# Optimization experiments

Measured on AMD Instinct MI355X. Metric: run time of the kernel, lower is better.

The kernel has to match this reference:

```python
import jax, jax.numpy as jnp
import numpy as np

K = 2  # top-k experts per token

def setup_inputs() -> dict:
    key = jax.random.key(0)
    ks = jax.random.split(key, 4)
    B, D, E, H = 8192, 512, 8, 2048
    x = jax.random.normal(ks[0], (B, D), dtype=jnp.float32)
    w_gate = jax.random.normal(ks[1], (D, E), dtype=jnp.float32) * 0.02
    W1 = jax.random.normal(ks[2], (E, D, H), dtype=jnp.float32) * (1.0 / np.sqrt(D))
    b1 = jnp.zeros((E, H), dtype=jnp.float32)
    W2 = jax.random.normal(ks[3], (E, H, D), dtype=jnp.float32) * (1.0 / np.sqrt(H))
    b2 = jnp.zeros((E, D), dtype=jnp.float32)
    return {"x": x, "w_gate": w_gate, "W1": W1, "b1": b1, "W2": W2, "b2": b2}

def reference(x, w_gate, W1, b1, W2, b2):
    B, E = x.shape[0], w_gate.shape[1]
    # --- gating (eval path: clean logits, no noise) ---
    logits = x @ w_gate                                  # [B, E]
    top_vals, top_idx = jax.lax.top_k(logits, K)         # [B, K]
    top_gates = jax.nn.softmax(top_vals, axis=-1)        # softmax over top-k logits
    rows = jnp.arange(B)[:, None]
    gates = jnp.zeros((B, E), dtype=x.dtype).at[rows, top_idx].set(top_gates)  # [B, E]
    # --- expert MLPs (grouped GEMMs) ---
    h = jax.nn.gelu(jnp.einsum('bd,edh->beh', x, W1) + b1[None], approximate=False)  # [B, E, H]
    out = jnp.einsum('beh,ehd->bed', h, W2) + b2[None]   # [B, E, D]
    # --- combine weighted by sparse gates ---
    y = jnp.einsum('be,bed->bd', gates, out)             # [B, D]
    return y
```

## Files before the change

kernel.cpp:

```cpp
#include <hip/hip_runtime.h>
#include <cstdint>

#define B_TOK 8192
#define DIM   512
#define NEXP  8
#define HID   2048

#define BM 128
#define BN 128
#define BK 64
#define BN2 64

typedef float  floatx4 __attribute__((ext_vector_type(4)));
typedef __bf16 bf16x8  __attribute__((ext_vector_type(8)));

__device__ __forceinline__ unsigned short f2bf(float f){
  unsigned u = __float_as_uint(f);
  u += 0x7fffu + ((u >> 16) & 1u);
  return (unsigned short)(u >> 16);
}

__device__ __forceinline__ float gelu_exact(float v){
  return 0.5f * v * (1.0f + erff(v * 0.70710678118654752440f));
}

__device__ __forceinline__ void async_load16(const void* g, void* l){
  __builtin_amdgcn_global_load_lds(
      (__attribute__((address_space(1))) unsigned int*)const_cast<void*>(g),
      (__attribute__((address_space(3))) unsigned int*)l, 16, 0, 0);
}


__global__ void k_cvt_x(const float* __restrict__ x, unsigned short* __restrict__ xb){
  int i = blockIdx.x * blockDim.x + threadIdx.x;
  float4 v = ((const float4*)x)[i];
  ushort4 o;
  o.x = f2bf(v.x); o.y = f2bf(v.y); o.z = f2bf(v.z); o.w = f2bf(v.w);
  ((ushort4*)xb)[i] = o;
}

__global__ __launch_bounds__(256)
void k_transpose_bf16(const float* __restrict__ src, unsigned short* __restrict__ dst,
                      int R, int C){
  __shared__ unsigned short tile[64][65];
  const size_t eoff = (size_t)blockIdx.z * (size_t)R * (size_t)C;
  const float* s = src + eoff;
  unsigned short* d = dst + eoff;
  int r0 = blockIdx.y * 64, c0 = blockIdx.x * 64;
  int tr = threadIdx.x >> 4, tc = threadIdx.x & 15;
  #pragma unroll
  for (int i = 0; i < 4; i++){
    int r = tr + i * 16;
    float4 v = *(const float4*)(s + (size_t)(r0 + r) * C + c0 + tc * 4);
    tile[tc*4+0][r] = f2bf(v.x);
    tile[tc*4+1][r] = f2bf(v.y);
    tile[tc*4+2][r] = f2bf(v.z);
    tile[tc*4+3][r] = f2bf(v.w);
  }
  __syncthreads();
  #pragma unroll
  for (int i = 0; i < 4; i++){
    int rr = tr + i * 16;
    ushort4 o;
    o.x = tile[rr][tc*4+0]; o.y = tile[rr][tc*4+1];
    o.z = tile[rr][tc*4+2]; o.w = tile[rr][tc*4+3];
    *(ushort4*)(d + (size_t)(c0 + rr) * R + r0 + tc * 4) = o;
  }
}

__global__ __launch_bounds__(256)
void k_gate(const float* __restrict__ x, const float* __restrict__ wg,
            int* __restrict__ tidx, float* __restrict__ tgate){
  const int wave = threadIdx.x >> 6, lane = threadIdx.x & 63;
  const int t = blockIdx.x * 4 + wave;
  const float* xr = x + (size_t)t * DIM;
  double acc[8];
  #pragma unroll
  for (int e = 0; e < 8; e++) acc[e] = 0.0;
  for (int d = lane; d < DIM; d += 64){
    double xv = (double)xr[d];
    float4 a = *(const float4*)(wg + d * 8);
    float4 b = *(const float4*)(wg + d * 8 + 4);
    acc[0] += xv * (double)a.x; acc[1] += xv * (double)a.y;
    acc[2] += xv * (double)a.z; acc[3] += xv * (double)a.w;
    acc[4] += xv * (double)b.x; acc[5] += xv * (double)b.y;
    acc[6] += xv * (double)b.z; acc[7] += xv * (double)b.w;
  }
  #pragma unroll
  for (int off = 32; off > 0; off >>= 1){
    #pragma unroll
    for (int e = 0; e < 8; e++)
      acc[e] += __shfl_down(acc[e], off);
  }
  if (lane == 0){
    int i0 = 0; double v0 = acc[0];
    #pragma unroll
    for (int e = 1; e < 8; e++) if (acc[e] > v0){ v0 = acc[e]; i0 = e; }
    int i1 = -1; double v1 = -1e300;
    #pragma unroll
    for (int e = 0; e < 8; e++) if (e != i0 && acc[e] > v1){ v1 = acc[e]; i1 = e; }
    double g0 = 1.0 / (1.0 + exp(v1 - v0));
    tidx[2*t]   = i0; tidx[2*t+1] = i1;
    tgate[2*t]  = (float)g0;
    tgate[2*t+1]= (float)(1.0 - g0);
  }
}

__global__ __launch_bounds__(1024)
void k_count(const int* __restrict__ tidx, int* __restrict__ ctrl){
  __shared__ int hist[16][8];
  const int tid = threadIdx.x;
  const int wave = tid >> 6;
  if (tid < 128) ((int*)hist)[tid] = 0;
  __syncthreads();
  #pragma unroll
  for (int i = 0; i < 8; i++){
    int t = i * 1024 + tid;
    int2 e = ((const int2*)tidx)[t];
    atomicAdd(&hist[wave][e.x], 1);
    atomicAdd(&hist[wave][e.y], 1);
  }
  __syncthreads();
  if (tid == 0){
    int o = 0;
    for (int e = 0; e < 8; e++){
      int c = 0;
      for (int w = 0; w < 16; w++) c += hist[w][e];
      ctrl[e] = c; ctrl[8 + e] = o; ctrl[16 + e] = o; o += c;
    }
  }
}

__global__ __launch_bounds__(256)
void k_place(const int* __restrict__ tidx, int* __restrict__ ctrl,
             int* __restrict__ perm, int2* __restrict__ slotpos){
  __shared__ int cnt[8];
  __shared__ int base[8];
  const int tid = threadIdx.x;
  if (tid < 8) cnt[tid] = 0;
  __syncthreads();
  const int t = blockIdx.x * 256 + tid;
  const int e0 = tidx[2*t], e1 = tidx[2*t+1];
  const int r0 = atomicAdd(&cnt[e0], 1);
  const int r1 = atomicAdd(&cnt[e1], 1);
  __syncthreads();
  if (tid < 8) base[tid] = atomicAdd(&ctrl[16 + tid], cnt[tid]);
  __syncthreads();
  const int p0 = base[e0] + r0, p1 = base[e1] + r1;
  perm[p0] = t;
  perm[p1] = t;
  slotpos[t] = make_int2(p0, p1);
}

__global__ __launch_bounds__(256, 2)
void k_gemm1(const unsigned short* __restrict__ xb,
             const unsigned short* __restrict__ w1t,
             const float* __restrict__ b1,
             unsigned short* __restrict__ h,
             const int* __restrict__ perm,
             const int* __restrict__ ctrl){
  const int e = blockIdx.z;
  const int count = ctrl[e];
  const int m0 = blockIdx.x * BM;
  if (m0 >= count) return;
  const int hoff = ctrl[8 + e];
  const int n0 = blockIdx.y * BN;

  __shared__ unsigned short smem[BM*BK + BN*BK + 2048];
  unsigned short* As = smem;
  unsigned short* Bs = smem + BM*BK;

  const int tid  = threadIdx.x;
  const int wave = tid >> 6;
  const int lane = tid & 63;
  const int rl   = wave * 32 + (lane >> 3);
  const int swz  = (lane & 7) ^ ((lane >> 3) & 7);

  const unsigned short* agp[4];
  const unsigned short* bgp[4];
  const unsigned short* w1e = w1t + (size_t)e * HID * DIM;
  #pragma unroll
  for (int i = 0; i < 4; i++){
    int mrow = m0 + rl + i * 8;
    int cl = mrow < count ? mrow : count - 1;
    int srow = perm[hoff + cl];
    agp[i] = xb + (size_t)srow * DIM + swz * 8;
    bgp[i] = w1e + (size_t)(n0 + rl + i * 8) * DIM + swz * 8;
  }
  unsigned short* asw = As + (wave * 32) * BK + lane * 8;
  unsigned short* bsw = Bs + (wave * 32) * BK + lane * 8;

  const int mh = (wave & 1) * 64;
  const int nh = (wave >> 1) * 64;
  const int fr = lane & 15;
  const int fq = lane >> 4;

  floatx4 acc[4][4];
  floatx4 zero = {0.f, 0.f, 0.f, 0.f};
  #pragma unroll
  for (int i = 0; i < 4; i++)
    #pragma unroll
    for (int j = 0; j < 4; j++) acc[i][j] = zero;

  for (int kt = 0; kt < DIM / BK; ++kt){
    #pragma unroll
    for (int i = 0; i < 4; i++){
      async_load16(agp[i] + kt * BK, asw + i * 8 * BK);
      async_load16(bgp[i] + kt * BK, bsw + i * 8 * BK);
    }
    __syncthreads();
    #pragma unroll
    for (int ks = 0; ks < 2; ks++){
      bf16x8 af[4], bfv[4];
      int kc = ks * 4 + fq;
      #pragma unroll
      for (int i = 0; i < 4; i++){
        int row = mh + i * 16 + fr;
        af[i] = *(const bf16x8*)(As + row * BK + ((kc ^ (row & 7)) << 3));
      }
      #pragma unroll
      for (int j = 0; j < 4; j++){
        int row = nh + j * 16 + fr;
        bfv[j] = *(const bf16x8*)(Bs + row * BK + ((kc ^ (row & 7)) << 3));
      }
      #pragma unroll
      for (int i = 0; i < 4; i++)
        #pragma unroll
        for (int j = 0; j < 4; j++)
          acc[i][j] = __builtin_amdgcn_mfma_f32_16x16x32_bf16(af[i], bfv[j], acc[i][j], 0, 0, 0);
    }
    __syncthreads();
  }

  unsigned short* wr = smem + wave * 4608;
  const int cm = fq * 4;
  const float* b1e = b1 + e * HID;
  #pragma unroll
  for (int i = 0; i < 4; i++){
    #pragma unroll
    for (int j = 0; j < 4; j++){
      float bias = b1e[n0 + nh + j * 16 + fr];
      #pragma unroll
      for (int r = 0; r < 4; r++){
        float v = acc[i][j][r] + bias;
        wr[(i * 16 + cm + r) * 72 + j * 16 + fr] = f2bf(gelu_exact(v));
      }
    }
  }
  __syncthreads();
  #pragma unroll
  for (int it = 0; it < 8; ++it){
    int row = it * 8 + (lane >> 3);
    int mrow = m0 + mh + row;
    if (mrow < count){
      uint4 vv = *(const uint4*)(wr + row * 72 + (lane & 7) * 8);
      *(uint4*)(h + (size_t)(hoff + mrow) * HID + n0 + nh + (lane & 7) * 8) = vv;
    }
  }
}

__global__ __launch_bounds__(256, 4)
void k_gemm2(const unsigned short* __restrict__ h,
             const unsigned short* __restrict__ w2t,
             float* __restrict__ slots,
             const int* __restrict__ ctrl){
  const int e = blockIdx.z;
  const int count = ctrl[e];
  const int m0 = blockIdx.x * BM;
  if (m0 >= count) return;
  const int hoff = ctrl[8 + e];
  const int n0 = blockIdx.y * BN2;

  __shared__ unsigned short smem[BM*BK + BN2*BK];
  unsigned short* As = smem;
  unsigned short* Bs = smem + BM*BK;

  const int tid  = threadIdx.x;
  const int wave = tid >> 6;
  const int lane = tid & 63;
  const int rl   = wave * 32 + (lane >> 3);
  const int rlb  = wave * 16 + (lane >> 3);
  const int swz  = (lane & 7) ^ ((lane >> 3) & 7);

  const unsigned short* agp[4];
  const unsigned short* bgp[2];
  const unsigned short* w2e = w2t + (size_t)e * DIM * HID;
  #pragma unroll
  for (int i = 0; i < 4; i++){
    agp[i] = h + (size_t)(hoff + m0 + rl + i * 8) * HID + swz * 8;
  }
  #pragma unroll
  for (int i = 0; i < 2; i++){
    bgp[i] = w2e + (size_t)(n0 + rlb + i * 8) * HID + swz * 8;
  }
  unsigned short* asw = As + (wave * 32) * BK + lane * 8;
  unsigned short* bsw = Bs + (wave * 16) * BK + lane * 8;

  const int mh  = (wave & 1) * 64;
  const int nh2 = (wave >> 1) * 32;
  const int fr = lane & 15;
  const int fq = lane >> 4;

  floatx4 acc[4][2];
  floatx4 zero = {0.f, 0.f, 0.f, 0.f};
  #pragma unroll
  for (int i = 0; i < 4; i++)
    #pragma unroll
    for (int j = 0; j < 2; j++) acc[i][j] = zero;

  for (int kt = 0; kt < HID / BK; ++kt){
    #pragma unroll
    for (int i = 0; i < 4; i++)
      async_load16(agp[i] + kt * BK, asw + i * 8 * BK);
    #pragma unroll
    for (int i = 0; i < 2; i++)
      async_load16(bgp[i] + kt * BK, bsw + i * 8 * BK);
    __syncthreads();
    #pragma unroll
    for (int ks = 0; ks < 2; ks++){
      bf16x8 af[4], bfv[2];
      int kc = ks * 4 + fq;
      #pragma unroll
      for (int i = 0; i < 4; i++){
        int row = mh + i * 16 + fr;
        af[i] = *(const bf16x8*)(As + row * BK + ((kc ^ (row & 7)) << 3));
      }
      #pragma unroll
      for (int j = 0; j < 2; j++){
        int row = nh2 + j * 16 + fr;
        bfv[j] = *(const bf16x8*)(Bs + row * BK + ((kc ^ (row & 7)) << 3));
      }
      #pragma unroll
      for (int i = 0; i < 4; i++)
        #pragma unroll
        for (int j = 0; j < 2; j++)
          acc[i][j] = __builtin_amdgcn_mfma_f32_16x16x32_bf16(af[i], bfv[j], acc[i][j], 0, 0, 0);
    }
    __syncthreads();
  }

  const int cm = fq * 4;
  #pragma unroll
  for (int i = 0; i < 4; i++){
    #pragma unroll
    for (int r = 0; r < 4; r++){
      int mrow = m0 + mh + i * 16 + cm + r;
      if (mrow < count){
        float* sr = slots + (size_t)(hoff + mrow) * DIM + n0 + nh2 + fr;
        #pragma unroll
        for (int j = 0; j < 2; j++)
          sr[j * 16] = acc[i][j][r];
      }
    }
  }
}

__global__ __launch_bounds__(256)
void k_combine(const float* __restrict__ slots, const int2* __restrict__ slotpos,
               const int* __restrict__ tidx, const float* __restrict__ tgate,
               const float* __restrict__ b2, float* __restrict__ y){
  const int idx = blockIdx.x * 256 + threadIdx.x;
  const int t  = idx >> 7;
  const int c4 = (idx & 127) * 4;
  int2 sp = slotpos[t];
  float4 o0 = *(const float4*)(slots + (size_t)sp.x * DIM + c4);
  float4 o1 = *(const float4*)(slots + (size_t)sp.y * DIM + c4);
  int   e0 = tidx[2*t],  e1 = tidx[2*t+1];
  float g0 = tgate[2*t], g1 = tgate[2*t+1];
  float4 bb0 = *(const float4*)(b2 + e0 * DIM + c4);
  float4 bb1 = *(const float4*)(b2 + e1 * DIM + c4);
  float4 r;
  r.x = g0 * (o0.x + bb0.x) + g1 * (o1.x + bb1.x);
  r.y = g0 * (o0.y + bb0.y) + g1 * (o1.y + bb1.y);
  r.z = g0 * (o0.z + bb0.z) + g1 * (o1.z + bb1.z);
  r.w = g0 * (o0.w + bb0.w) + g1 * (o1.w + bb1.w);
  *(float4*)(y + (size_t)t * DIM + c4) = r;
}

extern "C" void kernel_launch(void* const* d_in, const int* in_sizes, int n_in,
                              void* d_out, int out_size, void* d_ws, size_t ws_size,
                              hipStream_t stream){
  const float* x  = (const float*)d_in[0];
  const float* wg = (const float*)d_in[1];
  const float* W1 = (const float*)d_in[2];
  const float* b1 = (const float*)d_in[3];
  const float* W2 = (const float*)d_in[4];
  const float* b2 = (const float*)d_in[5];
  float* y = (float*)d_out;

  char* ws = (char*)d_ws;
  size_t off = 0;
  auto alloc = [&](size_t bytes) -> void* {
    void* p = ws + off;
    off = (off + bytes + 255) & ~(size_t)255;
    return p;
  };
  unsigned short* xb   = (unsigned short*)alloc((size_t)B_TOK * DIM * 2);
  unsigned short* w1t  = (unsigned short*)alloc((size_t)NEXP * HID * DIM * 2);
  float* slots = (float*)ws;
  unsigned short* w2t  = (unsigned short*)alloc((size_t)NEXP * DIM * HID * 2);
  unsigned short* hbuf = (unsigned short*)alloc((size_t)(2 * B_TOK + 128) * HID * 2);
  int*   perm    = (int*)  alloc((2 * B_TOK + 256) * 4);
  int2*  slotpos = (int2*) alloc((size_t)B_TOK * 8);
  int*   tidx  = (int*)  alloc(2 * B_TOK * 4);
  float* tgate = (float*)alloc(2 * B_TOK * 4);
  int*   ctrl  = (int*)  alloc(24 * 4);

  k_cvt_x<<<B_TOK * DIM / (256 * 4), 256, 0, stream>>>(x, xb);
  k_transpose_bf16<<<dim3(HID / 64, DIM / 64, NEXP), 256, 0, stream>>>(W1, w1t, DIM, HID);
  k_transpose_bf16<<<dim3(DIM / 64, HID / 64, NEXP), 256, 0, stream>>>(W2, w2t, HID, DIM);
  k_gate<<<B_TOK / 4, 256, 0, stream>>>(x, wg, tidx, tgate);
  k_count<<<1, 1024, 0, stream>>>(tidx, ctrl);
  k_place<<<B_TOK / 256, 256, 0, stream>>>(tidx, ctrl, perm, slotpos);
  k_gemm1<<<dim3(B_TOK / BM, HID / BN, NEXP), 256, 0, stream>>>(xb, w1t, b1, hbuf, perm, ctrl);
  k_gemm2<<<dim3(B_TOK / BM, DIM / BN2, NEXP), 256, 0, stream>>>(hbuf, w2t, slots, ctrl);
  k_combine<<<B_TOK * DIM / 4 / 256, 256, 0, stream>>>(slots, slotpos, tidx, tgate, b2, y);
}
```

Baseline: 339.4 us.

## Compact expert tile grid, fast erf GELU, bf16 slots, raise gemm1 occupancy

```diff
diff --git a/kernel.cpp b/kernel.cpp
--- a/kernel.cpp
+++ b/kernel.cpp
@@ -10,6 +10,8 @@
 #define BN 128
 #define BK 64
 #define BN2 64
+#define MAXTILES (B_TOK * 2 / BM + NEXP)
+#define PAD_SLOTS (MAXTILES * BM)
 
 typedef float  floatx4 __attribute__((ext_vector_type(4)));
 typedef __bf16 bf16x8  __attribute__((ext_vector_type(8)));
@@ -20,8 +22,21 @@
   return (unsigned short)(u >> 16);
 }
 
-__device__ __forceinline__ float gelu_exact(float v){
-  return 0.5f * v * (1.0f + erff(v * 0.70710678118654752440f));
+__device__ __forceinline__ float bf2f(unsigned short u){
+  return __uint_as_float((unsigned)u << 16);
+}
+
+__device__ __forceinline__ float erf_fast(float x){
+  float ax = fabsf(x);
+  float t  = 1.0f / (1.0f + 0.3275911f * ax);
+  float p  = t * (0.254829592f + t * (-0.284496736f + t * (1.421413741f +
+             t * (-1.453152027f + t * 1.061405429f))));
+  float r  = 1.0f - p * __expf(-ax * ax);
+  return copysignf(r, x);
+}
+
+__device__ __forceinline__ float gelu_fast(float v){
+  return 0.5f * v * (1.0f + erf_fast(v * 0.70710678118654752440f));
 }
 
 __device__ __forceinline__ void async_load16(const void* g, void* l){
@@ -107,7 +122,8 @@
 }
 
 __global__ __launch_bounds__(1024)
-void k_count(const int* __restrict__ tidx, int* __restrict__ ctrl){
+void k_count(const int* __restrict__ tidx, int* __restrict__ ctrl,
+             int2* __restrict__ tmap){
   __shared__ int hist[16][8];
   const int tid = threadIdx.x;
   const int wave = tid >> 6;
@@ -122,12 +138,16 @@
   }
   __syncthreads();
   if (tid == 0){
-    int o = 0;
+    int o = 0, nt = 0;
     for (int e = 0; e < 8; e++){
       int c = 0;
       for (int w = 0; w < 16; w++) c += hist[w][e];
-      ctrl[e] = c; ctrl[8 + e] = o; ctrl[16 + e] = o; o += c;
-    }
+      ctrl[e] = c; ctrl[8 + e] = o; ctrl[16 + e] = o;
+      int tiles = (c + BM - 1) / BM;
+      for (int tk = 0; tk < tiles; tk++) tmap[nt++] = make_int2(e, tk * BM);
+      o += tiles * BM;
+    }
+    for (; nt < MAXTILES; nt++) tmap[nt] = make_int2(0, 1 << 30);
   }
 }
 
@@ -152,16 +172,18 @@
   slotpos[t] = make_int2(p0, p1);
 }
 
-__global__ __launch_bounds__(256, 2)
+__global__ __launch_bounds__(256, 4)
 void k_gemm1(const unsigned short* __restrict__ xb,
              const unsigned short* __restrict__ w1t,
              const float* __restrict__ b1,
              unsigned short* __restrict__ h,
              const int* __restrict__ perm,
-             const int* __restrict__ ctrl){
-  const int e = blockIdx.z;
+             const int* __restrict__ ctrl,
+             const int2* __restrict__ tmap){
+  const int2 tm = tmap[blockIdx.x];
+  const int e = tm.x;
+  const int m0 = tm.y;
   const int count = ctrl[e];
-  const int m0 = blockIdx.x * BM;
   if (m0 >= count) return;
   const int hoff = ctrl[8 + e];
   const int n0 = blockIdx.y * BN;
@@ -181,9 +203,7 @@
   const unsigned short* w1e = w1t + (size_t)e * HID * DIM;
   #pragma unroll
   for (int i = 0; i < 4; i++){
-    int mrow = m0 + rl + i * 8;
-    int cl = mrow < count ? mrow : count - 1;
-    int srow = perm[hoff + cl];
+    int srow = perm[hoff + m0 + rl + i * 8];
     agp[i] = xb + (size_t)srow * DIM + swz * 8;
     bgp[i] = w1e + (size_t)(n0 + rl + i * 8) * DIM + swz * 8;
   }
@@ -243,7 +263,7 @@
       #pragma unroll
       for (int r = 0; r < 4; r++){
         float v = acc[i][j][r] + bias;
-        wr[(i * 16 + cm + r) * 72 + j * 16 + fr] = f2bf(gelu_exact(v));
+        wr[(i * 16 + cm + r) * 72 + j * 16 + fr] = f2bf(gelu_fast(v));
       }
     }
   }
@@ -262,11 +282,13 @@
 __global__ __launch_bounds__(256, 4)
 void k_gemm2(const unsigned short* __restrict__ h,
              const unsigned short* __restrict__ w2t,
-             float* __restrict__ slots,
-             const int* __restrict__ ctrl){
-  const int e = blockIdx.z;
+             unsigned short* __restrict__ slots,
+             const int* __restrict__ ctrl,
+             const int2* __restrict__ tmap){
+  const int2 tm = tmap[blockIdx.x];
+  const int e = tm.x;
+  const int m0 = tm.y;
   const int count = ctrl[e];
-  const int m0 = blockIdx.x * BM;
   if (m0 >= count) return;
   const int hoff = ctrl[8 + e];
   const int n0 = blockIdx.y * BN2;
@@ -346,34 +368,33 @@
     for (int r = 0; r < 4; r++){
       int mrow = m0 + mh + i * 16 + cm + r;
       if (mrow < count){
-        float* sr = slots + (size_t)(hoff + mrow) * DIM + n0 + nh2 + fr;
-        #pragma unroll
-        for (int j = 0; j < 2; j++)
-          sr[j * 16] = acc[i][j][r];
+        unsigned short* sr = slots + (size_t)(hoff + mrow) * DIM + n0 + nh2 + fr;
+        sr[0]  = f2bf(acc[i][0][r]);
+        sr[16] = f2bf(acc[i][1][r]);
       }
     }
   }
 }
 
 __global__ __launch_bounds__(256)
-void k_combine(const float* __restrict__ slots, const int2* __restrict__ slotpos,
+void k_combine(const unsigned short* __restrict__ slots, const int2* __restrict__ slotpos,
                const int* __restrict__ tidx, const float* __restrict__ tgate,
                const float* __restrict__ b2, float* __restrict__ y){
   const int idx = blockIdx.x * 256 + threadIdx.x;
   const int t  = idx >> 7;
   const int c4 = (idx & 127) * 4;
   int2 sp = slotpos[t];
-  float4 o0 = *(const float4*)(slots + (size_t)sp.x * DIM + c4);
-  float4 o1 = *(const float4*)(slots + (size_t)sp.y * DIM + c4);
+  ushort4 u0 = *(const ushort4*)(slots + (size_t)sp.x * DIM + c4);
+  ushort4 u1 = *(const ushort4*)(slots + (size_t)sp.y * DIM + c4);
   int   e0 = tidx[2*t],  e1 = tidx[2*t+1];
   float g0 = tgate[2*t], g1 = tgate[2*t+1];
   float4 bb0 = *(const float4*)(b2 + e0 * DIM + c4);
   float4 bb1 = *(const float4*)(b2 + e1 * DIM + c4);
   float4 r;
-  r.x = g0 * (o0.x + bb0.x) + g1 * (o1.x + bb1.x);
-  r.y = g0 * (o0.y + bb0.y) + g1 * (o1.y + bb1.y);
-  r.z = g0 * (o0.z + bb0.z) + g1 * (o1.z + bb1.z);
-  r.w = g0 * (o0.w + bb0.w) + g1 * (o1.w + bb1.w);
+  r.x = g0 * (bf2f(u0.x) + bb0.x) + g1 * (bf2f(u1.x) + bb1.x);
+  r.y = g0 * (bf2f(u0.y) + bb0.y) + g1 * (bf2f(u1.y) + bb1.y);
+  r.z = g0 * (bf2f(u0.z) + bb0.z) + g1 * (bf2f(u1.z) + bb1.z);
+  r.w = g0 * (bf2f(u0.w) + bb0.w) + g1 * (bf2f(u1.w) + bb1.w);
   *(float4*)(y + (size_t)t * DIM + c4) = r;
 }
 
@@ -397,22 +418,27 @@
   };
   unsigned short* xb   = (unsigned short*)alloc((size_t)B_TOK * DIM * 2);
   unsigned short* w1t  = (unsigned short*)alloc((size_t)NEXP * HID * DIM * 2);
-  float* slots = (float*)ws;
+  unsigned short* slots = (unsigned short*)ws;
+  static_assert((size_t)PAD_SLOTS * DIM * 2 <= (size_t)B_TOK * DIM * 2 + (size_t)NEXP * HID * DIM * 2,
+                "slots must fit in dead xb+w1t region");
   unsigned short* w2t  = (unsigned short*)alloc((size_t)NEXP * DIM * HID * 2);
-  unsigned short* hbuf = (unsigned short*)alloc((size_t)(2 * B_TOK + 128) * HID * 2);
-  int*   perm    = (int*)  alloc((2 * B_TOK + 256) * 4);
+  unsigned short* hbuf = (unsigned short*)alloc((size_t)PAD_SLOTS * HID * 2);
+  int*   perm    = (int*)  alloc((size_t)PAD_SLOTS * 4);
   int2*  slotpos = (int2*) alloc((size_t)B_TOK * 8);
+  int2*  tmap    = (int2*) alloc(MAXTILES * 8);
   int*   tidx  = (int*)  alloc(2 * B_TOK * 4);
   float* tgate = (float*)alloc(2 * B_TOK * 4);
   int*   ctrl  = (int*)  alloc(24 * 4);
+
+  hipMemsetAsync(perm, 0, (size_t)PAD_SLOTS * 4, stream);
 
   k_cvt_x<<<B_TOK * DIM / (256 * 4), 256, 0, stream>>>(x, xb);
   k_transpose_bf16<<<dim3(HID / 64, DIM / 64, NEXP), 256, 0, stream>>>(W1, w1t, DIM, HID);
   k_transpose_bf16<<<dim3(DIM / 64, HID / 64, NEXP), 256, 0, stream>>>(W2, w2t, HID, DIM);
   k_gate<<<B_TOK / 4, 256, 0, stream>>>(x, wg, tidx, tgate);
-  k_count<<<1, 1024, 0, stream>>>(tidx, ctrl);
+  k_count<<<1, 1024, 0, stream>>>(tidx, ctrl, tmap);
   k_place<<<B_TOK / 256, 256, 0, stream>>>(tidx, ctrl, perm, slotpos);
-  k_gemm1<<<dim3(B_TOK / BM, HID / BN, NEXP), 256, 0, stream>>>(xb, w1t, b1, hbuf, perm, ctrl);
-  k_gemm2<<<dim3(B_TOK / BM, DIM / BN2, NEXP), 256, 0, stream>>>(hbuf, w2t, slots, ctrl);
+  k_gemm1<<<dim3(MAXTILES, HID / BN), 256, 0, stream>>>(xb, w1t, b1, hbuf, perm, ctrl, tmap);
+  k_gemm2<<<dim3(MAXTILES, DIM / BN2), 256, 0, stream>>>(hbuf, w2t, slots, ctrl, tmap);
   k_combine<<<B_TOK * DIM / 4 / 256, 256, 0, stream>>>(slots, slotpos, tidx, tgate, b2, y);
 }
```

New measurement: 309.8 us. -8.7%, faster.
